# Kernel tuning notes

Measured on AMD Instinct MI355X. Metric: run time of the kernel, lower is better.

## Reference

```python
import jax, jax.numpy as jnp
import numpy as np

N = 50000            # nodes
E = 800000           # random edges (self loops added in reference, per PyG default)
D_IN, D1, D2, D_OUT = 256, 128, 64, 40
SLOPE = 0.2          # GATv2Conv default negative_slope


def _glorot(key, shape):
    fan_in, fan_out = shape[0], shape[-1]
    s = jnp.sqrt(6.0 / (fan_in + fan_out))
    return jax.random.uniform(key, shape, jnp.float32, -s, s)


def setup_inputs() -> dict:
    key = jax.random.key(0)
    ks = jax.random.split(key, 16)
    inp = {
        "x": jax.random.normal(ks[0], (N, D_IN), jnp.float32),
        "edge_index": jax.random.randint(ks[1], (2, E), 0, N),
    }
    dims = [(D_IN, D1), (D1, D2), (D2, D_OUT)]
    k = 2
    for i, (di, do) in enumerate(dims, 1):
        inp[f"W{i}l"] = _glorot(ks[k], (di, do)); k += 1
        inp[f"W{i}r"] = _glorot(ks[k], (di, do)); k += 1
        inp[f"b{i}l"] = jnp.zeros((do,), jnp.float32)
        inp[f"b{i}r"] = jnp.zeros((do,), jnp.float32)
        inp[f"a{i}"]  = _glorot(ks[k], (do,));    k += 1
        inp[f"c{i}"]  = jnp.zeros((do,), jnp.float32)
    return inp


def _gatv2(x, src, dst, Wl, bl, Wr, br, att, bias):
    # GATv2Conv, heads=1: lin_l on source nodes, lin_r on target nodes
    xl = x @ Wl + bl                     # [N, do] source transform
    xr = x @ Wr + br                     # [N, do] target transform
    e = jax.nn.leaky_relu(xl[src] + xr[dst], SLOPE)   # [Etot, do]
    logits = e @ att                     # [Etot]
    # segment softmax over incoming edges of each dst node
    m = jax.ops.segment_max(logits, dst, num_segments=N)
    ex = jnp.exp(logits - m[dst])
    denom = jax.ops.segment_sum(ex, dst, num_segments=N)
    alpha = ex / denom[dst]              # [Etot]
    out = jax.ops.segment_sum(alpha[:, None] * xl[src], dst, num_segments=N)
    return out + bias


def reference(x, edge_index,
              W1l, W1r, b1l, b1r, a1, c1,
              W2l, W2r, b2l, b2r, a2, c2,
              W3l, W3r, b3l, b3r, a3, c3):
    loop = jnp.arange(N, dtype=edge_index.dtype)
    src = jnp.concatenate([edge_index[0], loop])   # add_self_loops=True
    dst = jnp.concatenate([edge_index[1], loop])
    h = jax.nn.relu(_gatv2(x, src, dst, W1l, b1l, W1r, b1r, a1, c1))
    h = jax.nn.relu(_gatv2(h, src, dst, W2l, b2l, W2r, b2r, a2, c2))
    h = _gatv2(h, src, dst, W3l, b3l, W3r, b3r, a3, c3)
    return jax.nn.log_softmax(h, axis=1)
```

## Files before the change

### kernel.cpp

```cpp
#include <hip/hip_runtime.h>
#include <math.h>

#define NN 50000
#define NE 800000
#define SLOPE 0.2f
#define NEGX (-1e30f)
#define CH 8192

typedef _Float16 h8 __attribute__((ext_vector_type(8)));
typedef _Float16 h2 __attribute__((ext_vector_type(2)));
typedef float f8 __attribute__((ext_vector_type(8)));
typedef float v4f __attribute__((ext_vector_type(4)));

__device__ __forceinline__ h8 hzero(){ h8 z = {0,0,0,0,0,0,0,0}; return z; }

__device__ __forceinline__ void pack_one(const float* __restrict__ W,
                                         _Float16* __restrict__ Wp,
                                         int DO, int K, int NT, int t){
  int KC = K >> 5;
  if (t >= NT * KC * 64) return;
  int lane = t & 63;
  int rest = t >> 6;
  int c  = rest % KC;
  int nt = rest / KC;
  int col = nt * 16 + (lane & 15);
  int k0  = c * 32 + ((lane >> 4) << 3);
  _Float16 o[8];
#pragma unroll
  for (int j = 0; j < 8; j++){
    float v = (col < DO) ? W[(k0 + j) * DO + col] : 0.f;
    o[j] = (_Float16)v;
  }
  *(ulonglong2*)(Wp + (size_t)t * 8) = *(ulonglong2*)o;
}

__global__ __launch_bounds__(256) void k_pack_hist(
    const float* W1l, const float* W1r, const float* W2l,
    const float* W2r, const float* W3l, const float* W3r,
    _Float16* p1l, _Float16* p1r, _Float16* p2l,
    _Float16* p2r, _Float16* p3l, _Float16* p3r,
    const int* __restrict__ ei, int* __restrict__ gbp){
  __shared__ int h[256];
  int b = blockIdx.x, t = threadIdx.x;
  if (b < 44){
    if      (b < 16) pack_one(W1l, p1l, 128, 256, 8, (b     ) * 256 + t);
    else if (b < 32) pack_one(W1r, p1r, 128, 256, 8, (b - 16) * 256 + t);
    else if (b < 36) pack_one(W2l, p2l,  64, 128, 4, (b - 32) * 256 + t);
    else if (b < 40) pack_one(W2r, p2r,  64, 128, 4, (b - 36) * 256 + t);
    else if (b < 42) pack_one(W3l, p3l,  40,  64, 3, (b - 40) * 256 + t);
    else             pack_one(W3r, p3r,  40,  64, 3, (b - 42) * 256 + t);
  } else {
    int hb = b - 44;
    h[t] = 0;
    __syncthreads();
    int e0 = hb * 12500;
    for (int i = t; i < 12500; i += 256)
      atomicAdd(&h[ei[NE + e0 + i] >> 8], 1);
    __syncthreads();
    gbp[hb * 256 + t] = h[t];
  }
}

__global__ __launch_bounds__(256) void k_scan(const int* __restrict__ gbp,
                                              int* __restrict__ base,
                                              int* __restrict__ bcur,
                                              int* __restrict__ row_ptr){
  __shared__ int s[256];
  int t = threadIdx.x;
  int v = 0;
#pragma unroll 8
  for (int i = 0; i < 64; i++) v += gbp[i * 256 + t];
  s[t] = v; __syncthreads();
  for (int off = 1; off < 256; off <<= 1){
    int a = (t >= off) ? s[t - off] : 0;
    __syncthreads(); s[t] += a; __syncthreads();
  }
  int ex = s[t] - v;
  base[t] = ex;
  bcur[t] = ex;
  if (t == 255){ base[256] = s[255]; row_ptr[NN] = s[255]; }
}

__global__ __launch_bounds__(256) void k_bscatter(const int* __restrict__ ei,
                                                  int* __restrict__ bcur,
                                                  unsigned* __restrict__ pk_out){
  __shared__ unsigned pk[CH];
  __shared__ int h[256];
  int t = threadIdx.x;
  int e0 = blockIdx.x * CH;
  h[t] = 0;
  __syncthreads();
  int n = NE - e0; if (n > CH) n = CH;
  for (int i = t; i < n; i += 256){
    int e = e0 + i;
    int s = ei[e], d = ei[NE + e];
    pk[i] = (unsigned)s | ((unsigned)(d & 255) << 16) | ((unsigned)(d >> 8) << 24);
    atomicAdd(&h[d >> 8], 1);
  }
  __syncthreads();
  int c = h[t];
  if (c) h[t] = atomicAdd(&bcur[t], c);
  __syncthreads();
  for (int i = t; i < n; i += 256){
    unsigned u = pk[i];
    int pos = atomicAdd(&h[u >> 24], 1);
    pk_out[pos] = u;
  }
}

__global__ __launch_bounds__(256) void k_bcsr(const unsigned* __restrict__ pk,
                                              const int* __restrict__ base,
                                              int* __restrict__ row_ptr,
                                              int* __restrict__ csr_src){
  __shared__ int h[256], s[256];
  int t = threadIdx.x;
  int b = blockIdx.x;
  int lo = base[b], hi = base[b + 1];
  h[t] = 0;
  __syncthreads();
  for (int i = lo + t; i < hi; i += 256)
    atomicAdd(&h[(pk[i] >> 16) & 255], 1);
  __syncthreads();
  int v = h[t];
  s[t] = v; __syncthreads();
  for (int off = 1; off < 256; off <<= 1){
    int a = (t >= off) ? s[t - off] : 0;
    __syncthreads(); s[t] += a; __syncthreads();
  }
  int ex = lo + s[t] - v;
  int node = b * 256 + t;
  if (node < NN) row_ptr[node] = ex;
  h[t] = ex;
  __syncthreads();
  for (int i = lo + t; i < hi; i += 256){
    unsigned u = pk[i];
    int pos = atomicAdd(&h[(u >> 16) & 255], 1);
    csr_src[pos] = (int)(u & 0xFFFFu);
  }
}

template<typename TI, int K, int DO>
__global__ __launch_bounds__(256, 4) void gemm_direct(
    const TI* __restrict__ X,
    const _Float16* __restrict__ Wpl, const float* __restrict__ bl,
    const _Float16* __restrict__ Wpr, const float* __restrict__ br,
    _Float16* __restrict__ Yl, _Float16* __restrict__ Yr)
{
  constexpr int KC = K / 32;
  constexpr int NT = (DO + 15) / 16;
  int lane = threadIdx.x & 63;
  int wv   = threadIdx.x >> 6;
  int row0 = (blockIdx.x * 4 + wv) * 16;
  int arow = lane & 15;
  int koff = lane >> 4;
  int lrow = row0 + arow;
  int crow = (lrow < NN) ? lrow : 0;

  h8 afrag[KC];
  if constexpr (sizeof(TI) == 4){
    const float* Xr = (const float*)X + (size_t)crow * K + koff * 8;
#pragma unroll
    for (int c = 0; c < KC; c++){
      float4 v0 = *reinterpret_cast<const float4*>(Xr + c * 32);
      float4 v1 = *reinterpret_cast<const float4*>(Xr + c * 32 + 4);
      h8 a;
      a[0]=(_Float16)v0.x; a[1]=(_Float16)v0.y; a[2]=(_Float16)v0.z; a[3]=(_Float16)v0.w;
      a[4]=(_Float16)v1.x; a[5]=(_Float16)v1.y; a[6]=(_Float16)v1.z; a[7]=(_Float16)v1.w;
      afrag[c] = a;
    }
  } else {
    const _Float16* Xr = (const _Float16*)X + (size_t)crow * K + koff * 8;
#pragma unroll
    for (int c = 0; c < KC; c++)
      afrag[c] = *reinterpret_cast<const h8*>(Xr + c * 32);
  }

#pragma unroll
  for (int side = 0; side < 2; side++){
    const _Float16* Wp = side ? Wpr : Wpl;
    const float* bias = side ? br : bl;
    _Float16* Y = side ? Yr : Yl;
#pragma unroll
    for (int nt = 0; nt < NT; nt++){
      v4f acc = {0.f, 0.f, 0.f, 0.f};
#pragma unroll
      for (int c = 0; c < KC; c++){
        h8 b = *reinterpret_cast<const h8*>(Wp + (size_t)((nt * KC + c) * 64 + lane) * 8);
        acc = __builtin_amdgcn_mfma_f32_16x16x32_f16(afrag[c], b, acc, 0, 0, 0);
      }
      int col = nt * 16 + arow;
      if (col < DO){
        float bv = bias[col];
        int rbase = row0 + koff * 4;
#pragma unroll
        for (int r = 0; r < 4; r++){
          int orow = rbase + r;
          if (orow < NN) Y[(size_t)orow * DO + col] = (_Float16)(acc[r] + bv);
        }
      }
    }
  }
}

__device__ __forceinline__ float edge_logit(h8 x, h8 xrv, h8 attv){
  h8 t = x + xrv;
  h8 l = __builtin_elementwise_max(t, t * (_Float16)SLOPE);
  const h2* lp = (const h2*)&l;
  const h2* ap = (const h2*)&attv;
  h2 d = lp[0] * ap[0];
  d += lp[1] * ap[1];
  d += lp[2] * ap[2];
  d += lp[3] * ap[3];
  return (float)d[0] + (float)d[1];
}

template<int LPG>
__device__ __forceinline__ float gsum(float v){
#pragma unroll
  for (int off = 1; off < LPG; off <<= 1) v += __shfl_xor(v, off, 64);
  return v;
}
template<int LPG>
__device__ __forceinline__ void gsum2(float& a, float& b){
#pragma unroll
  for (int off = 1; off < LPG; off <<= 1){
    a += __shfl_xor(a, off, 64);
    b += __shfl_xor(b, off, 64);
  }
}
template<int LPG>
__device__ __forceinline__ float gmax(float v){
#pragma unroll
  for (int off = 1; off < LPG; off <<= 1) v = fmaxf(v, __shfl_xor(v, off, 64));
  return v;
}

template<int DO, int LPG, int DO2>
__global__ __launch_bounds__(256) void agg_gemm(
    const _Float16* __restrict__ xl, const _Float16* __restrict__ xr,
    const int* __restrict__ csr_src, const int* __restrict__ row_ptr,
    const float* __restrict__ att, const float* __restrict__ bias,
    const _Float16* __restrict__ Wpl2, const float* __restrict__ bl2,
    const _Float16* __restrict__ Wpr2, const float* __restrict__ br2,
    _Float16* __restrict__ Yl, _Float16* __restrict__ Yr)
{
  constexpr int G = 64 / LPG;
  constexpr int NPB = 4 * G;
  constexpr int LK = DO + 8;
  constexpr int KC2 = DO / 32;
  constexpr int NT2 = (DO2 + 15) / 16;
  constexpr int MT = NPB / 16;
  __shared__ _Float16 hs[NPB * LK];

  int lane = threadIdx.x & 63;
  int wid  = threadIdx.x >> 6;
  int g = lane / LPG, p = lane % LPG;
  int nodeLocal = wid * G + g;
  int node = blockIdx.x * NPB + nodeLocal;
  int cbase = p * 8;
  bool nvalid = node < NN;
  int nodeC = nvalid ? node : 0;

  h8 attv, xrv, xlv;
  {
    float4 a0 = *reinterpret_cast<const float4*>(att + cbase);
    float4 a1 = *reinterpret_cast<const float4*>(att + cbase + 4);
    attv[0]=(_Float16)a0.x; attv[1]=(_Float16)a0.y; attv[2]=(_Float16)a0.z; attv[3]=(_Float16)a0.w;
    attv[4]=(_Float16)a1.x; attv[5]=(_Float16)a1.y; attv[6]=(_Float16)a1.z; attv[7]=(_Float16)a1.w;
    xrv = *reinterpret_cast<const h8*>(xr + nodeC * DO + cbase);
    xlv = *reinterpret_cast<const h8*>(xl + nodeC * DO + cbase);
  }
  float s = gsum<LPG>(edge_logit(xlv, xrv, attv));
  float wS = __expf(s);
  float denA = wS, denB = 0.f;
  float accA[8], accB[8];
  {
    f8 xf = __builtin_convertvector(xlv, f8);
#pragma unroll
    for (int j = 0; j < 8; j++){ accA[j] = wS * xf[j]; accB[j] = 0.f; }
  }

  int e0 = row_ptr[nodeC];
  int e1 = nvalid ? row_ptr[nodeC + 1] : e0;
  int e = e0;
  for (; e + 1 < e1; e += 2){
    int sA = csr_src[e], sB = csr_src[e + 1];
    h8 xA = *reinterpret_cast<const h8*>(xl + sA * DO + cbase);
    h8 xB = *reinterpret_cast<const h8*>(xl + sB * DO + cbase);
    float pA = edge_logit(xA, xrv, attv);
    float pB = edge_logit(xB, xrv, attv);
    gsum2<LPG>(pA, pB);
    float wA = __expf(pA), wB = __expf(pB);
    denA += wA; denB += wB;
    f8 fA = __builtin_convertvector(xA, f8);
    f8 fB = __builtin_convertvector(xB, f8);
#pragma unroll
    for (int j = 0; j < 8; j++){
      accA[j] = fmaf(wA, fA[j], accA[j]);
      accB[j] = fmaf(wB, fB[j], accB[j]);
    }
  }
  if (e < e1){
    int sA = csr_src[e];
    h8 xA = *reinterpret_cast<const h8*>(xl + sA * DO + cbase);
    float pA = gsum<LPG>(edge_logit(xA, xrv, attv));
    float w = __expf(pA);
    denA += w;
    f8 fA = __builtin_convertvector(xA, f8);
#pragma unroll
    for (int j = 0; j < 8; j++) accA[j] = fmaf(w, fA[j], accA[j]);
  }

  {
    float inv = 1.0f / (denA + denB);
    f8 vv;
#pragma unroll
    for (int j = 0; j < 8; j++)
      vv[j] = fmaxf(fmaf(accA[j] + accB[j], inv, bias[cbase + j]), 0.f);
    h8 ho = __builtin_convertvector(vv, h8);
    *reinterpret_cast<h8*>(&hs[nodeLocal * LK + cbase]) = ho;
  }
  __syncthreads();

  int arow = lane & 15;
  int koff = lane >> 4;
  int mt = (MT == 1) ? 0 : (wid >> 1);
  h8 afrag[KC2];
#pragma unroll
  for (int c = 0; c < KC2; c++)
    afrag[c] = *reinterpret_cast<const h8*>(&hs[(mt * 16 + arow) * LK + koff * 8 + c * 32]);

  int row0 = blockIdx.x * NPB + mt * 16;
  int side = wid & 1;
  const _Float16* Wp = side ? Wpr2 : Wpl2;
  const float* bias2 = side ? br2 : bl2;
  _Float16* Y = side ? Yr : Yl;
  int nt_begin = (MT == 1) ? (wid >> 1) * (NT2 / 2) : 0;
  int nt_end   = (MT == 1) ? nt_begin + NT2 / 2 : NT2;
  for (int nt = nt_begin; nt < nt_end; nt++){
    v4f acc = {0.f, 0.f, 0.f, 0.f};
#pragma unroll
    for (int c = 0; c < KC2; c++){
      h8 b = *reinterpret_cast<const h8*>(Wp + (size_t)((nt * KC2 + c) * 64 + lane) * 8);
      acc = __builtin_amdgcn_mfma_f32_16x16x32_f16(afrag[c], b, acc, 0, 0, 0);
    }
    int col = nt * 16 + arow;
    if (col < DO2){
      float bv = bias2[col];
      int rbase = row0 + koff * 4;
#pragma unroll
      for (int r = 0; r < 4; r++){
        int orow = rbase + r;
        if (orow < NN) Y[(size_t)orow * DO2 + col] = (_Float16)(acc[r] + bv);
      }
    }
  }
}

template<int DO, int LPG>
__global__ __launch_bounds__(256) void gat_agg_out(
    const _Float16* __restrict__ xl, const _Float16* __restrict__ xr,
    const int* __restrict__ csr_src, const int* __restrict__ row_ptr,
    const float* __restrict__ att, const float* __restrict__ bias,
    float* __restrict__ out)
{
  constexpr int G = 64 / LPG;
  int lane = threadIdx.x & 63;
  int wv = (blockIdx.x * 256 + threadIdx.x) >> 6;
  int g = lane / LPG;
  int p = lane % LPG;
  int node = wv * G + g;
  if (node >= NN) return;
  int cbase = p * 8;
  bool ok = (cbase < DO);

  h8 attv = hzero(), xrv = hzero(), xlv = hzero();
  if (ok){
    float4 a0 = *reinterpret_cast<const float4*>(att + cbase);
    float4 a1 = *reinterpret_cast<const float4*>(att + cbase + 4);
    attv[0]=(_Float16)a0.x; attv[1]=(_Float16)a0.y; attv[2]=(_Float16)a0.z; attv[3]=(_Float16)a0.w;
    attv[4]=(_Float16)a1.x; attv[5]=(_Float16)a1.y; attv[6]=(_Float16)a1.z; attv[7]=(_Float16)a1.w;
    xrv = *reinterpret_cast<const h8*>(xr + node * DO + cbase);
    xlv = *reinterpret_cast<const h8*>(xl + node * DO + cbase);
  }

  float s = gsum<LPG>(edge_logit(xlv, xrv, attv));
  float wS = __expf(s);
  float denA = wS, denB = 0.f;
  float accA[8], accB[8];
  {
    f8 xf = __builtin_convertvector(xlv, f8);
#pragma unroll
    for (int j = 0; j < 8; j++){ accA[j] = wS * xf[j]; accB[j] = 0.f; }
  }

  int e0 = row_ptr[node], e1 = row_ptr[node + 1];
  int e = e0;
  for (; e + 1 < e1; e += 2){
    int sA = csr_src[e], sB = csr_src[e + 1];
    h8 xA = ok ? *reinterpret_cast<const h8*>(xl + sA * DO + cbase) : hzero();
    h8 xB = ok ? *reinterpret_cast<const h8*>(xl + sB * DO + cbase) : hzero();
    float pA = edge_logit(xA, xrv, attv);
    float pB = edge_logit(xB, xrv, attv);
    gsum2<LPG>(pA, pB);
    float wA = __expf(pA), wB = __expf(pB);
    denA += wA; denB += wB;
    f8 fA = __builtin_convertvector(xA, f8);
    f8 fB = __builtin_convertvector(xB, f8);
#pragma unroll
    for (int j = 0; j < 8; j++){
      accA[j] = fmaf(wA, fA[j], accA[j]);
      accB[j] = fmaf(wB, fB[j], accB[j]);
    }
  }
  if (e < e1){
    int sA = csr_src[e];
    h8 xA = ok ? *reinterpret_cast<const h8*>(xl + sA * DO + cbase) : hzero();
    float pA = gsum<LPG>(edge_logit(xA, xrv, attv));
    float w = __expf(pA);
    denA += w;
    f8 fA = __builtin_convertvector(xA, f8);
#pragma unroll
    for (int j = 0; j < 8; j++) accA[j] = fmaf(w, fA[j], accA[j]);
  }

  float inv = 1.0f / (denA + denB);
  float v[8]; float lmax = NEGX;
#pragma unroll
  for (int j = 0; j < 8; j++){
    v[j] = ok ? fmaf(accA[j] + accB[j], inv, bias[cbase + j]) : NEGX;
    lmax = fmaxf(lmax, v[j]);
  }
  lmax = gmax<LPG>(lmax);
  float lsum = 0.f;
#pragma unroll
  for (int j = 0; j < 8; j++) lsum += __expf(v[j] - lmax);
  lsum = gsum<LPG>(lsum);
  if (ok){
    float lg = lmax + __logf(lsum);
    float* op = (float*)out + node * DO + cbase;
    float4 o0, o1;
    o0.x = v[0] - lg; o0.y = v[1] - lg; o0.z = v[2] - lg; o0.w = v[3] - lg;
    o1.x = v[4] - lg; o1.y = v[5] - lg; o1.z = v[6] - lg; o1.w = v[7] - lg;
    *reinterpret_cast<float4*>(op) = o0;
    *reinterpret_cast<float4*>(op + 4) = o1;
  }
}

extern "C" void kernel_launch(void* const* d_in, const int* in_sizes, int n_in,
                              void* d_out, int out_size, void* d_ws, size_t ws_size,
                              hipStream_t stream) {
  const float* x   = (const float*)d_in[0];
  const int*   ei  = (const int*)d_in[1];
  const float* W1l = (const float*)d_in[2];  const float* W1r = (const float*)d_in[3];
  const float* b1l = (const float*)d_in[4];  const float* b1r = (const float*)d_in[5];
  const float* a1  = (const float*)d_in[6];  const float* c1  = (const float*)d_in[7];
  const float* W2l = (const float*)d_in[8];  const float* W2r = (const float*)d_in[9];
  const float* b2l = (const float*)d_in[10]; const float* b2r = (const float*)d_in[11];
  const float* a2  = (const float*)d_in[12]; const float* c2  = (const float*)d_in[13];
  const float* W3l = (const float*)d_in[14]; const float* W3r = (const float*)d_in[15];
  const float* b3l = (const float*)d_in[16]; const float* b3r = (const float*)d_in[17];
  const float* a3  = (const float*)d_in[18]; const float* c3  = (const float*)d_in[19];
  float* outp = (float*)d_out;

  _Float16* xl1 = (_Float16*)d_ws;
  _Float16* xr1 = xl1 + 6400000;
  _Float16* xl2 = xr1 + 6400000;
  _Float16* xr2 = xl2 + 3200000;
  _Float16* xl3 = xr2 + 3200000;
  _Float16* xr3 = xl3 + 2000000;
  _Float16* wp1l = xr3 + 2000000;
  _Float16* wp1r = wp1l + 32768;
  _Float16* wp2l = wp1r + 32768;
  _Float16* wp2r = wp2l + 8192;
  _Float16* wp3l = wp2r + 8192;
  _Float16* wp3r = wp3l + 3072;
  unsigned* pk   = (unsigned*)(wp3r + 3072);
  int* csr_src   = (int*)(pk + NE);
  int* row_ptr   = csr_src + NE;
  int* gbp       = row_ptr + 50001;
  int* base      = gbp + 16384;
  int* bcur      = base + 257;

  const int GB = (NN + 63) / 64;
  const int SB = (NE + CH - 1) / CH;
  const int FB1 = (NN + 15) / 16;
  const int FB2 = (NN + 31) / 32;
  const int AB3 = (NN + 31) / 32;

  k_pack_hist<<<108, 256, 0, stream>>>(W1l, W1r, W2l, W2r, W3l, W3r,
                                       wp1l, wp1r, wp2l, wp2r, wp3l, wp3r,
                                       ei, gbp);
  k_scan<<<1, 256, 0, stream>>>(gbp, base, bcur, row_ptr);
  k_bscatter<<<SB, 256, 0, stream>>>(ei, bcur, pk);
  k_bcsr<<<196, 256, 0, stream>>>(pk, base, row_ptr, csr_src);

  gemm_direct<float,256,128><<<GB, 256, 0, stream>>>(x, wp1l, b1l, wp1r, b1r, xl1, xr1);

  agg_gemm<128,16,64><<<FB1, 256, 0, stream>>>(xl1, xr1, csr_src, row_ptr,
                                               a1, c1, wp2l, b2l, wp2r, b2r, xl2, xr2);

  agg_gemm<64,8,40><<<FB2, 256, 0, stream>>>(xl2, xr2, csr_src, row_ptr,
                                             a2, c2, wp3l, b3l, wp3r, b3r, xl3, xr3);

  gat_agg_out<40,8><<<AB3, 256, 0, stream>>>(xl3, xr3, csr_src, row_ptr, a3, c3, outp);
}
```

Before: 286.9 us.

## Sort nodes by in-degree so aggregation wavefronts process similar-degree nodes

Builds a degree histogram during CSR construction, scans it, and scatters nodes into a degree-sorted permutation. The aggregation and fused GEMM kernels then map node groups via this permutation, so lanes in a wavefront handle nodes with matching edge counts and less work is lost to divergence. This adds two small kernels plus an indirection per node. Output rows are written in scattered order, and neighbouring nodes no longer share a block, which can hurt the locality of xr/xl reads.

```diff
diff --git a/kernel.cpp b/kernel.cpp
--- a/kernel.cpp
+++ b/kernel.cpp
@@ -64,9 +64,11 @@
 __global__ __launch_bounds__(256) void k_scan(const int* __restrict__ gbp,
                                               int* __restrict__ base,
                                               int* __restrict__ bcur,
-                                              int* __restrict__ row_ptr){
+                                              int* __restrict__ row_ptr,
+                                              int* __restrict__ dhist){
   __shared__ int s[256];
   int t = threadIdx.x;
+  if (t < 64) dhist[t] = 0;
   int v = 0;
 #pragma unroll 8
   for (int i = 0; i < 64; i++) v += gbp[i * 256 + t];
@@ -111,12 +113,14 @@
 __global__ __launch_bounds__(256) void k_bcsr(const unsigned* __restrict__ pk,
                                               const int* __restrict__ base,
                                               int* __restrict__ row_ptr,
-                                              int* __restrict__ csr_src){
-  __shared__ int h[256], s[256];
+                                              int* __restrict__ csr_src,
+                                              int* __restrict__ dhist){
+  __shared__ int h[256], s[256], dh[64];
   int t = threadIdx.x;
   int b = blockIdx.x;
   int lo = base[b], hi = base[b + 1];
   h[t] = 0;
+  if (t < 64) dh[t] = 0;
   __syncthreads();
   for (int i = lo + t; i < hi; i += 256)
     atomicAdd(&h[(pk[i] >> 16) & 255], 1);
@@ -129,14 +133,51 @@
   }
   int ex = lo + s[t] - v;
   int node = b * 256 + t;
-  if (node < NN) row_ptr[node] = ex;
+  if (node < NN){
+    row_ptr[node] = ex;
+    atomicAdd(&dh[v < 63 ? v : 63], 1);
+  }
   h[t] = ex;
   __syncthreads();
+  if (t < 64 && dh[t]) atomicAdd(&dhist[t], dh[t]);
   for (int i = lo + t; i < hi; i += 256){
     unsigned u = pk[i];
     int pos = atomicAdd(&h[(u >> 16) & 255], 1);
     csr_src[pos] = (int)(u & 0xFFFFu);
   }
+}
+
+__global__ __launch_bounds__(64) void k_dscan(const int* __restrict__ dhist,
+                                              int* __restrict__ dcur){
+  __shared__ int s[64];
+  int t = threadIdx.x;
+  int v = dhist[t];
+  s[t] = v; __syncthreads();
+  for (int off = 1; off < 64; off <<= 1){
+    int a = (t >= off) ? s[t - off] : 0;
+    __syncthreads(); s[t] += a; __syncthreads();
+  }
+  dcur[t] = s[t] - v;
+}
+
+__global__ __launch_bounds__(256) void k_dscatter(const int* __restrict__ row_ptr,
+                                                  int* __restrict__ dcur,
+                                                  int* __restrict__ perm){
+  __shared__ int dh[64];
+  int t = threadIdx.x;
+  int node = blockIdx.x * 256 + t;
+  int bin = -1, rank = 0;
+  if (t < 64) dh[t] = 0;
+  __syncthreads();
+  if (node < NN){
+    int deg = row_ptr[node + 1] - row_ptr[node];
+    bin = deg < 63 ? deg : 63;
+    rank = atomicAdd(&dh[bin], 1);
+  }
+  __syncthreads();
+  if (t < 64){ int c = dh[t]; dh[t] = c ? atomicAdd(&dcur[t], c) : 0; }
+  __syncthreads();
+  if (bin >= 0) perm[dh[bin] + rank] = node;
 }
 
 template<typename TI, int K, int DO>
@@ -235,10 +276,50 @@
   return v;
 }
 
+template<int DO, int LPG, bool MASK>
+__device__ __forceinline__ void agg_edges(
+    const _Float16* __restrict__ xl, const int* __restrict__ csr_src,
+    int e0, int e1, int cbase, bool ok, h8 xrv, h8 attv,
+    float& denA, float& denB, float* accA, float* accB)
+{
+  int e = e0;
+  for (; e + 1 < e1; e += 2){
+    int sA = csr_src[e], sB = csr_src[e + 1];
+    h8 xA, xB;
+    if (!MASK || ok){
+      xA = *reinterpret_cast<const h8*>(xl + sA * DO + cbase);
+      xB = *reinterpret_cast<const h8*>(xl + sB * DO + cbase);
+    } else { xA = hzero(); xB = hzero(); }
+    float pA = edge_logit(xA, xrv, attv);
+    float pB = edge_logit(xB, xrv, attv);
+    gsum2<LPG>(pA, pB);
+    float wA = __expf(pA), wB = __expf(pB);
+    denA += wA; denB += wB;
+    f8 fA = __builtin_convertvector(xA, f8);
+    f8 fB = __builtin_convertvector(xB, f8);
+#pragma unroll
+    for (int j = 0; j < 8; j++){
+      accA[j] = fmaf(wA, fA[j], accA[j]);
+      accB[j] = fmaf(wB, fB[j], accB[j]);
+    }
+  }
+  if (e < e1){
+    int sA = csr_src[e];
+    h8 xA = (!MASK || ok) ? *reinterpret_cast<const h8*>(xl + sA * DO + cbase) : hzero();
+    float pA = gsum<LPG>(edge_logit(xA, xrv, attv));
+    float w = __expf(pA);
+    denA += w;
+    f8 fA = __builtin_convertvector(xA, f8);
+#pragma unroll
+    for (int j = 0; j < 8; j++) accA[j] = fmaf(w, fA[j], accA[j]);
+  }
+}
+
 template<int DO, int LPG, int DO2>
 __global__ __launch_bounds__(256) void agg_gemm(
     const _Float16* __restrict__ xl, const _Float16* __restrict__ xr,
     const int* __restrict__ csr_src, const int* __restrict__ row_ptr,
+    const int* __restrict__ perm,
     const float* __restrict__ att, const float* __restrict__ bias,
     const _Float16* __restrict__ Wpl2, const float* __restrict__ bl2,
     const _Float16* __restrict__ Wpr2, const float* __restrict__ br2,
@@ -251,15 +332,18 @@
   constexpr int NT2 = (DO2 + 15) / 16;
   constexpr int MT = NPB / 16;
   __shared__ _Float16 hs[NPB * LK];
+  __shared__ int pn[NPB];
 
   int lane = threadIdx.x & 63;
   int wid  = threadIdx.x >> 6;
   int g = lane / LPG, p = lane % LPG;
   int nodeLocal = wid * G + g;
-  int node = blockIdx.x * NPB + nodeLocal;
+  int idx = blockIdx.x * NPB + nodeLocal;
   int cbase = p * 8;
+  int node = (idx < NN) ? perm[idx] : NN;
   bool nvalid = node < NN;
   int nodeC = nvalid ? node : 0;
+  if (p == 0) pn[nodeLocal] = node;
 
   h8 attv, xrv, xlv;
   {
@@ -282,41 +366,15 @@
 
   int e0 = row_ptr[nodeC];
   int e1 = nvalid ? row_ptr[nodeC + 1] : e0;
-  int e = e0;
-  for (; e + 1 < e1; e += 2){
-    int sA = csr_src[e], sB = csr_src[e + 1];
-    h8 xA = *reinterpret_cast<const h8*>(xl + sA * DO + cbase);
-    h8 xB = *reinterpret_cast<const h8*>(xl + sB * DO + cbase);
-    float pA = edge_logit(xA, xrv, attv);
-    float pB = edge_logit(xB, xrv, attv);
-    gsum2<LPG>(pA, pB);
-    float wA = __expf(pA), wB = __expf(pB);
-    denA += wA; denB += wB;
-    f8 fA = __builtin_convertvector(xA, f8);
-    f8 fB = __builtin_convertvector(xB, f8);
-#pragma unroll
-    for (int j = 0; j < 8; j++){
-      accA[j] = fmaf(wA, fA[j], accA[j]);
-      accB[j] = fmaf(wB, fB[j], accB[j]);
-    }
-  }
-  if (e < e1){
-    int sA = csr_src[e];
-    h8 xA = *reinterpret_cast<const h8*>(xl + sA * DO + cbase);
-    float pA = gsum<LPG>(edge_logit(xA, xrv, attv));
-    float w = __expf(pA);
-    denA += w;
-    f8 fA = __builtin_convertvector(xA, f8);
-#pragma unroll
-    for (int j = 0; j < 8; j++) accA[j] = fmaf(w, fA[j], accA[j]);
-  }
+  agg_edges<DO, LPG, false>(xl, csr_src, e0, e1, cbase, true, xrv, attv,
+                            denA, denB, accA, accB);
 
   {
-    float inv = 1.0f / (denA + denB);
+    float inv = nvalid ? 1.0f / (denA + denB) : 0.f;
     f8 vv;
 #pragma unroll
     for (int j = 0; j < 8; j++)
-      vv[j] = fmaxf(fmaf(accA[j] + accB[j], inv, bias[cbase + j]), 0.f);
+      vv[j] = nvalid ? fmaxf(fmaf(accA[j] + accB[j], inv, bias[cbase + j]), 0.f) : 0.f;
     h8 ho = __builtin_convertvector(vv, h8);
     *reinterpret_cast<h8*>(&hs[nodeLocal * LK + cbase]) = ho;
   }
@@ -330,28 +388,28 @@
   for (int c = 0; c < KC2; c++)
     afrag[c] = *reinterpret_cast<const h8*>(&hs[(mt * 16 + arow) * LK + koff * 8 + c * 32]);
 
-  int row0 = blockIdx.x * NPB + mt * 16;
   int side = wid & 1;
   const _Float16* Wp = side ? Wpr2 : Wpl2;
   const float* bias2 = side ? br2 : bl2;
   _Float16* Y = side ? Yr : Yl;
   int nt_begin = (MT == 1) ? (wid >> 1) * (NT2 / 2) : 0;
   int nt_end   = (MT == 1) ? nt_begin + NT2 / 2 : NT2;
+  int prow[4];
+#pragma unroll
+  for (int r = 0; r < 4; r++) prow[r] = pn[mt * 16 + koff * 4 + r];
   for (int nt = nt_begin; nt < nt_end; nt++){
-    v4f acc = {0.f, 0.f, 0.f, 0.f};
+    v4f acc2 = {0.f, 0.f, 0.f, 0.f};
 #pragma unroll
     for (int c = 0; c < KC2; c++){
       h8 b = *reinterpret_cast<const h8*>(Wp + (size_t)((nt * KC2 + c) * 64 + lane) * 8);
-      acc = __builtin_amdgcn_mfma_f32_16x16x32_f16(afrag[c], b, acc, 0, 0, 0);
+      acc2 = __builtin_amdgcn_mfma_f32_16x16x32_f16(afrag[c], b, acc2, 0, 0, 0);
     }
     int col = nt * 16 + arow;
     if (col < DO2){
       float bv = bias2[col];
-      int rbase = row0 + koff * 4;
 #pragma unroll
       for (int r = 0; r < 4; r++){
-        int orow = rbase + r;
-        if (orow < NN) Y[(size_t)orow * DO2 + col] = (_Float16)(acc[r] + bv);
+        if (prow[r] < NN) Y[(size_t)prow[r] * DO2 + col] = (_Float16)(acc2[r] + bv);
       }
     }
   }
@@ -361,6 +419,7 @@
 __global__ __launch_bounds__(256) void gat_agg_out(
     const _Float16* __restrict__ xl, const _Float16* __restrict__ xr,
     const int* __restrict__ csr_src, const int* __restrict__ row_ptr,
+    const int* __restrict__ perm,
     const float* __restrict__ att, const float* __restrict__ bias,
     float* __restrict__ out)
 {
@@ -369,8 +428,9 @@
   int wv = (blockIdx.x * 256 + threadIdx.x) >> 6;
   int g = lane / LPG;
   int p = lane % LPG;
-  int node = wv * G + g;
-  if (node >= NN) return;
+  int idx = wv * G + g;
+  if (idx >= NN) return;
+  int node = perm[idx];
   int cbase = p * 8;
   bool ok = (cbase < DO);
 
@@ -395,34 +455,8 @@
   }
 
   int e0 = row_ptr[node], e1 = row_ptr[node + 1];
-  int e = e0;
-  for (; e + 1 < e1; e += 2){
-    int sA = csr_src[e], sB = csr_src[e + 1];
-    h8 xA = ok ? *reinterpret_cast<const h8*>(xl + sA * DO + cbase) : hzero();
-    h8 xB = ok ? *reinterpret_cast<const h8*>(xl + sB * DO + cbase) : hzero();
-    float pA = edge_logit(xA, xrv, attv);
-    float pB = edge_logit(xB, xrv, attv);
-    gsum2<LPG>(pA, pB);
-    float wA = __expf(pA), wB = __expf(pB);
-    denA += wA; denB += wB;
-    f8 fA = __builtin_convertvector(xA, f8);
-    f8 fB = __builtin_convertvector(xB, f8);
-#pragma unroll
-    for (int j = 0; j < 8; j++){
-      accA[j] = fmaf(wA, fA[j], accA[j]);
-      accB[j] = fmaf(wB, fB[j], accB[j]);
-    }
-  }
-  if (e < e1){
-    int sA = csr_src[e];
-    h8 xA = ok ? *reinterpret_cast<const h8*>(xl + sA * DO + cbase) : hzero();
-    float pA = gsum<LPG>(edge_logit(xA, xrv, attv));
-    float w = __expf(pA);
-    denA += w;
-    f8 fA = __builtin_convertvector(xA, f8);
-#pragma unroll
-    for (int j = 0; j < 8; j++) accA[j] = fmaf(w, fA[j], accA[j]);
-  }
+  agg_edges<DO, LPG, true>(xl, csr_src, e0, e1, cbase, ok, xrv, attv,
+                           denA, denB, accA, accB);
 
   float inv = 1.0f / (denA + denB);
   float v[8]; float lmax = NEGX;
@@ -438,7 +472,7 @@
   lsum = gsum<LPG>(lsum);
   if (ok){
     float lg = lmax + __logf(lsum);
-    float* op = (float*)out + node * DO + cbase;
+    float* op = (float*)out + (size_t)node * DO + cbase;
     float4 o0, o1;
     o0.x = v[0] - lg; o0.y = v[1] - lg; o0.z = v[2] - lg; o0.w = v[3] - lg;
     o1.x = v[4] - lg; o1.y = v[5] - lg; o1.z = v[6] - lg; o1.w = v[7] - lg;
@@ -481,9 +515,13 @@
   int* gbp       = row_ptr + 50001;
   int* base      = gbp + 16384;
   int* bcur      = base + 257;
+  int* dhist     = bcur + 256;
+  int* dcur      = dhist + 64;
+  int* perm      = dcur + 64;
 
   const int GB = (NN + 63) / 64;
   const int SB = (NE + CH - 1) / CH;
+  const int NB = (NN + 255) / 256;
   const int FB1 = (NN + 15) / 16;
   const int FB2 = (NN + 31) / 32;
   const int AB3 = (NN + 31) / 32;
@@ -491,17 +529,20 @@
   k_pack_hist<<<108, 256, 0, stream>>>(W1l, W1r, W2l, W2r, W3l, W3r,
                                        wp1l, wp1r, wp2l, wp2r, wp3l, wp3r,
                                        ei, gbp);
-  k_scan<<<1, 256, 0, stream>>>(gbp, base, bcur, row_ptr);
+  k_scan<<<1, 256, 0, stream>>>(gbp, base, bcur, row_ptr, dhist);
   k_bscatter<<<SB, 256, 0, stream>>>(ei, bcur, pk);
-  k_bcsr<<<196, 256, 0, stream>>>(pk, base, row_ptr, csr_src);
+  k_bcsr<<<NB, 256, 0, stream>>>(pk, base, row_ptr, csr_src, dhist);
+  k_dscan<<<1, 64, 0, stream>>>(dhist, dcur);
+  k_dscatter<<<NB, 256, 0, stream>>>(row_ptr, dcur, perm);
 
   gemm_direct<float,256,128><<<GB, 256, 0, stream>>>(x, wp1l, b1l, wp1r, b1r, xl1, xr1);
 
-  agg_gemm<128,16,64><<<FB1, 256, 0, stream>>>(xl1, xr1, csr_src, row_ptr,
+  agg_gemm<128,16,64><<<FB1, 256, 0, stream>>>(xl1, xr1, csr_src, row_ptr, perm,
                                                a1, c1, wp2l, b2l, wp2r, b2r, xl2, xr2);
 
-  agg_gemm<64,8,40><<<FB2, 256, 0, stream>>>(xl2, xr2, csr_src, row_ptr,
+  agg_gemm<64,8,40><<<FB2, 256, 0, stream>>>(xl2, xr2, csr_src, row_ptr, perm,
                                              a2, c2, wp3l, b3l, wp3r, b3r, xl3, xr3);
 
-  gat_agg_out<40,8><<<AB3, 256, 0, stream>>>(xl3, xr3, csr_src, row_ptr, a3, c3, outp);
-}
+  gat_agg_out<40,8><<<AB3, 256, 0, stream>>>(xl3, xr3, csr_src, row_ptr, perm,
+                                             a3, c3, outp);
+}
```

Result: slower. 296.4 us (+3.3%).
